# Optimization experiments

Hardware: AMD Instinct MI355X
Metric: run time of the kernel (lower is better)

The kernel has to match this reference:

```python
import jax, jax.numpy as jnp
import numpy as np

NUM_EXPERTS = 8
TOP_K = 2
N_EMBD = 1024
D_FFN = 2048  # 4*n_embd//top_k, already multiple of block_size=128


def setup_inputs() -> dict:
    key = jax.random.key(0)
    k1, k2, k3, k4 = jax.random.split(key, 4)
    x = jax.random.normal(k1, (4, 2048, N_EMBD), dtype=jnp.float32)
    router_w = jax.random.normal(k2, (NUM_EXPERTS, N_EMBD), dtype=jnp.float32) * 0.02
    w1 = jax.random.normal(k3, (N_EMBD, D_FFN * NUM_EXPERTS), dtype=jnp.float32) * 0.02
    w2 = jax.random.normal(k4, (D_FFN * NUM_EXPERTS, N_EMBD), dtype=jnp.float32) * 0.02
    return {"x": x, "router_w": router_w, "w1": w1, "w2": w2}


def reference(x, router_w, w1, w2):
    B, T, D = x.shape
    xf = x.reshape(B * T, D)                       # [N, d]
    N = B * T

    # Router: softmax over experts, then top-k selection and renormalization.
    logits = xf @ router_w.T                       # [N, E]
    probs = jax.nn.softmax(logits, axis=-1)
    top_v, top_i = jax.lax.top_k(probs, TOP_K)     # [N, k]
    top_v = top_v / jnp.sum(top_v, axis=-1, keepdims=True)  # norm_topk_prob=True

    # Dense [N, E] routing-weight matrix (zero for non-selected experts).
    gate = jnp.zeros((N, NUM_EXPERTS), dtype=x.dtype)
    gate = gate.at[jnp.arange(N)[:, None], top_i].set(top_v)

    w1r = w1.reshape(D, NUM_EXPERTS, D_FFN)        # expert-major column blocks
    w2r = w2.reshape(NUM_EXPERTS, D_FFN, D)

    out = jnp.zeros((N, D), dtype=x.dtype)
    for e in range(NUM_EXPERTS):
        h = jax.nn.gelu(xf @ w1r[:, e, :], approximate=False)  # [N, f]
        out = out + gate[:, e:e + 1] * (h @ w2r[e])
    return out.reshape(B, T, D)
```

## Files before the change

### kernel.cpp

```cpp
#include <hip/hip_runtime.h>
#include <hip/hip_bf16.h>
#include <cstdint>
#include <cstddef>

#define NE 8
#define N_TOK 8192
#define D_EMB 1024
#define D_FFN 2048

#define BM 128
#define BN 128
#define BK 32

typedef __attribute__((ext_vector_type(8))) short short8;
typedef __attribute__((ext_vector_type(4))) float f32x4;

__device__ __forceinline__ unsigned short f2bf(float f) {
  union { float f; unsigned int u; } c; c.f = f;
  unsigned int u = c.u;
  unsigned int r = u + 0x7FFFu + ((u >> 16) & 1u);
  return (unsigned short)(r >> 16);
}

__device__ __forceinline__ float bf2f(unsigned short u) {
  union { unsigned int u; float f; } c; c.u = ((unsigned int)u) << 16;
  return c.f;
}

__device__ __forceinline__ float gelu_f(float x) {
  float u = x * x * x * 0.044715f + x;
  float t = __expf(-1.5957691216057308f * u);
  return x * __builtin_amdgcn_rcpf(1.f + t);
}

__device__ __forceinline__ void gll16(const void* g, void* l) {
  __builtin_amdgcn_global_load_lds((const __attribute__((address_space(1))) void*)g,
                                   (__attribute__((address_space(3))) void*)l, 16, 0, 0);
}

#define SB() __builtin_amdgcn_sched_barrier(0)
#define VW(N) { asm volatile("s_waitcnt vmcnt(" #N ")" ::: "memory"); SB(); }
#define BAR() { SB(); __builtin_amdgcn_s_barrier(); SB(); }
#define LKW() { asm volatile("s_waitcnt lgkmcnt(0)" ::: "memory"); SB(); }

__global__ __launch_bounds__(256) void router_k(const float* __restrict__ x,
                                                const float* __restrict__ rw,
                                                int* __restrict__ ti,
                                                float* __restrict__ tg,
                                                ushort* __restrict__ xb) {
  int w = threadIdx.x >> 6, lane = threadIdx.x & 63;
  int n = blockIdx.x * 4 + w;
  const float4* x4 = (const float4*)(x + (size_t)n * D_EMB);
  ushort4* xb4 = (ushort4*)(xb + (size_t)n * D_EMB);
  const float4* r4 = (const float4*)rw;
  float acc[NE];
#pragma unroll
  for (int e = 0; e < NE; ++e) acc[e] = 0.f;
#pragma unroll
  for (int c = 0; c < 4; ++c) {
    float4 xv = x4[c * 64 + lane];
    ushort4 o;
    o.x = f2bf(xv.x); o.y = f2bf(xv.y); o.z = f2bf(xv.z); o.w = f2bf(xv.w);
    xb4[c * 64 + lane] = o;
#pragma unroll
    for (int e = 0; e < NE; ++e) {
      float4 wv = r4[e * 256 + c * 64 + lane];
      acc[e] += xv.x * wv.x + xv.y * wv.y + xv.z * wv.z + xv.w * wv.w;
    }
  }
#pragma unroll
  for (int e = 0; e < NE; ++e) {
    float v = acc[e];
#pragma unroll
    for (int off = 32; off >= 1; off >>= 1) v += __shfl_xor(v, off);
    acc[e] = v;
  }
  if (lane == 0) {
    int e0 = 0; float v0 = acc[0];
#pragma unroll
    for (int e = 1; e < NE; ++e) if (acc[e] > v0) { v0 = acc[e]; e0 = e; }
    int e1 = -1; float v1 = -1e30f;
#pragma unroll
    for (int e = 0; e < NE; ++e) if (e != e0 && acc[e] > v1) { v1 = acc[e]; e1 = e; }
    float p1 = expf(v1 - v0);
    float g0 = 1.f / (1.f + p1);
    float g1 = p1 * g0;
    ti[2 * n] = e0; ti[2 * n + 1] = e1;
    tg[2 * n] = g0; tg[2 * n + 1] = g1;
  }
}

__global__ __launch_bounds__(256) void prep_k(const float* __restrict__ w1,
                                              const float* __restrict__ w2,
                                              const int* __restrict__ ti,
                                              ushort* __restrict__ w1t,
                                              ushort* __restrict__ w2te,
                                              int* __restrict__ counts) {
  int b = blockIdx.x;
  if (b >= 32768) {
    __shared__ int lc[NE];
    if (threadIdx.x < NE) lc[threadIdx.x] = 0;
    __syncthreads();
    int s = (b - 32768) * 512 + threadIdx.x;
    atomicAdd(&lc[ti[s]], 1);
    atomicAdd(&lc[ti[s + 256]], 1);
    __syncthreads();
    if (threadIdx.x < NE) atomicAdd(&counts[threadIdx.x], lc[threadIdx.x]);
    return;
  }
  __shared__ ushort t[32][33];
  int rl = threadIdx.x >> 3, q = threadIdx.x & 7;
  if (b < 16384) {
    int bx = b & 511, by = b >> 9;
    const int C = NE * D_FFN;
    float4 v = *(const float4*)&w1[(size_t)(by * 32 + rl) * C + bx * 32 + q * 4];
    t[rl][q * 4 + 0] = f2bf(v.x);
    t[rl][q * 4 + 1] = f2bf(v.y);
    t[rl][q * 4 + 2] = f2bf(v.z);
    t[rl][q * 4 + 3] = f2bf(v.w);
    __syncthreads();
    ushort4 o;
    o.x = t[q * 4 + 0][rl];
    o.y = t[q * 4 + 1][rl];
    o.z = t[q * 4 + 2][rl];
    o.w = t[q * 4 + 3][rl];
    *(ushort4*)&w1t[(size_t)(bx * 32 + rl) * D_EMB + by * 32 + q * 4] = o;
  } else {
    int b2 = b - 16384;
    int bx = b2 & 31, by = b2 >> 5;
    float4 v = *(const float4*)&w2[(size_t)(by * 32 + rl) * D_EMB + bx * 32 + q * 4];
    t[rl][q * 4 + 0] = f2bf(v.x);
    t[rl][q * 4 + 1] = f2bf(v.y);
    t[rl][q * 4 + 2] = f2bf(v.z);
    t[rl][q * 4 + 3] = f2bf(v.w);
    __syncthreads();
    int e = by >> 6;
    int f0 = (by & 63) * 32;
    size_t eoff = (size_t)e * (D_EMB * D_FFN);
    ushort4 o;
    o.x = t[q * 4 + 0][rl];
    o.y = t[q * 4 + 1][rl];
    o.z = t[q * 4 + 2][rl];
    o.w = t[q * 4 + 3][rl];
    *(ushort4*)&w2te[eoff + (size_t)(bx * 32 + rl) * D_FFN + f0 + q * 4] = o;
  }
}

__global__ void prefix_k(const int* __restrict__ counts, int* __restrict__ bases,
                         int* __restrict__ cursor) {
  if (threadIdx.x == 0) {
    int s = 0;
    for (int e = 0; e < NE; ++e) { bases[e] = s; cursor[e] = s; s += counts[e]; }
  }
}

__global__ __launch_bounds__(256) void scatter_k(const int* __restrict__ ti,
                                                 const float* __restrict__ tg,
                                                 int* __restrict__ cursor,
                                                 int* __restrict__ tokS,
                                                 float* __restrict__ gate) {
  __shared__ int lc[NE], lb[NE];
  if (threadIdx.x < NE) lc[threadIdx.x] = 0;
  __syncthreads();
  int s = blockIdx.x * 256 + threadIdx.x;
  int e = ti[s];
  float g = tg[s];
  int loc = atomicAdd(&lc[e], 1);
  __syncthreads();
  if (threadIdx.x < NE) lb[threadIdx.x] = atomicAdd(&cursor[threadIdx.x], lc[threadIdx.x]);
  __syncthreads();
  int pos = lb[e] + loc;
  tokS[pos] = s;
  gate[pos] = g;
}


#define STG(BUF)                                                           \
  { _Pragma("unroll") for (int j_ = 0; j_ < 2; ++j_) {                     \
      gll16(aptr[j_], &Al[BUF][ldso[j_]]);                                 \
      gll16(bptr[j_], &Bl[BUF][ldso[j_]]);                                 \
      aptr[j_] += BK; bptr[j_] += BK;                                      \
    } }

#define CMP(BUF)                                                           \
  { short8 a[4], b[4];                                                     \
    _Pragma("unroll") for (int i_ = 0; i_ < 4; ++i_)                       \
      a[i_] = *(const short8*)&Al[BUF][arow + i_ * 16 * BK];               \
    _Pragma("unroll") for (int j_ = 0; j_ < 4; ++j_)                       \
      b[j_] = *(const short8*)&Bl[BUF][brow + j_ * 16 * BK];               \
    _Pragma("unroll") for (int i_ = 0; i_ < 4; ++i_)                       \
      _Pragma("unroll") for (int j_ = 0; j_ < 4; ++j_)                     \
        acc[i_][j_] = __builtin_amdgcn_mfma_f32_16x16x32_bf16(a[i_], b[j_], acc[i_][j_], 0, 0, 0); \
  }

#define KLOOP(NT)                                                          \
  STG(0);                                                                  \
  for (int ks = 0; ks < (NT) - 2; ks += 2) {                               \
    STG(1); VW(4); BAR(); CMP(0); BAR();                                   \
    STG(0); VW(4); BAR(); CMP(1); BAR();                                   \
  }                                                                        \
  STG(1); VW(4); BAR(); CMP(0); BAR();                                     \
  VW(0); BAR(); CMP(1);

__global__ __launch_bounds__(256) void gemm1_k(const ushort* __restrict__ xb,
                                               const ushort* __restrict__ w1t,
                                               const int* __restrict__ counts,
                                               const int* __restrict__ bases,
                                               const int* __restrict__ tokS,
                                               ushort* __restrict__ h) {
  int bid = (int)blockIdx.x;
  bid = (bid & 7) * 512 + (bid >> 3);
  int e = bid >> 9;
  int rem = bid & 511;
  int mt = rem >> 4, nt = rem & 15;
  int count = counts[e];
  if (mt * BM >= count) return;
  int base = bases[e];

  __shared__ ushort Al[2][BM * BK];
  __shared__ ushort Bl[2][BN * BK];

  int tid = threadIdx.x;
  int w = tid >> 6, lane = tid & 63;

  const int ssw = (((lane & 3) ^ ((lane >> 3) & 3))) * 8;

  const ushort* aptr[2]; const ushort* bptr[2];
  int ldso[2];
#pragma unroll
  for (int j = 0; j < 2; ++j) {
    int rl = w * 32 + j * 16 + (lane >> 2);
    int pr = min(base + mt * BM + rl, base + count - 1);
    int t = tokS[pr] >> 1;
    aptr[j] = xb + (size_t)t * D_EMB + ssw;
    int c = e * D_FFN + nt * BN + rl;
    bptr[j] = w1t + (size_t)c * D_EMB + ssw;
    ldso[j] = (w * 32 + j * 16) * BK;
  }

  f32x4 zero = {0.f, 0.f, 0.f, 0.f};
  f32x4 acc[4][4];
#pragma unroll
  for (int i = 0; i < 4; ++i)
#pragma unroll
    for (int j = 0; j < 4; ++j) acc[i][j] = zero;

  int wm = w >> 1, wn = w & 1;
  const int rsw = ((lane >> 4) ^ (((lane & 15) >> 1) & 3)) * 8;
  const int arow = (wm * 64 + (lane & 15)) * BK + rsw;
  const int brow = (wn * 64 + (lane & 15)) * BK + rsw;

  KLOOP(D_EMB / BK);

  __syncthreads();
  ushort* ep = &Bl[0][0] + w * (16 * 72);
  int r0 = mt * BM + wm * 64, c0 = nt * BN + wn * 64;
  const int l15 = lane & 15;
#pragma unroll
  for (int i = 0; i < 4; ++i) {
#pragma unroll
    for (int j = 0; j < 4; ++j)
#pragma unroll
      for (int q = 0; q < 4; ++q)
        ep[((lane >> 4) * 4 + q) * 72 + j * 16 + l15] = f2bf(gelu_f(acc[i][j][q]));
    LKW();
#pragma unroll
    for (int rd = 0; rd < 2; ++rd) {
      int sr = (lane >> 3) + rd * 8;
      int sc = (lane & 7) * 8;
      short8 v = *(const short8*)&ep[sr * 72 + sc];
      int row = r0 + i * 16 + sr;
      if (row < count)
        *(short8*)&h[(size_t)(base + row) * D_FFN + c0 + sc] = v;
    }
    LKW();
  }
}

__global__ __launch_bounds__(256) void gemm2_k(const ushort* __restrict__ h,
                                               const ushort* __restrict__ w2te,
                                               const int* __restrict__ counts,
                                               const int* __restrict__ bases,
                                               const int* __restrict__ tokS,
                                               const float* __restrict__ gate,
                                               ushort* __restrict__ y2) {
  int bid = (int)blockIdx.x;
  bid = (bid & 7) * 256 + (bid >> 3);
  int e = bid >> 8;
  int rem = bid & 255;
  int mt = rem >> 3, nt = rem & 7;
  int count = counts[e];
  if (mt * BM >= count) return;
  int base = bases[e];

  __shared__ ushort Al[2][BM * BK];
  __shared__ ushort Bl[2][BN * BK];

  int tid = threadIdx.x;
  int w = tid >> 6, lane = tid & 63;

  const int ssw = (((lane & 3) ^ ((lane >> 3) & 3))) * 8;

  const ushort* aptr[2]; const ushort* bptr[2];
  int ldso[2];
#pragma unroll
  for (int j = 0; j < 2; ++j) {
    int rl = w * 32 + j * 16 + (lane >> 2);
    int pr = min(base + mt * BM + rl, base + count - 1);
    aptr[j] = h + (size_t)pr * D_FFN + ssw;
    int d = nt * BN + rl;
    bptr[j] = w2te + (size_t)e * (D_EMB * D_FFN) + (size_t)d * D_FFN + ssw;
    ldso[j] = (w * 32 + j * 16) * BK;
  }

  f32x4 zero = {0.f, 0.f, 0.f, 0.f};
  f32x4 acc[4][4];
#pragma unroll
  for (int i = 0; i < 4; ++i)
#pragma unroll
    for (int j = 0; j < 4; ++j) acc[i][j] = zero;

  int wm = w >> 1, wn = w & 1;
  const int rsw = ((lane >> 4) ^ (((lane & 15) >> 1) & 3)) * 8;
  const int arow = (wm * 64 + (lane & 15)) * BK + rsw;
  const int brow = (wn * 64 + (lane & 15)) * BK + rsw;

  KLOOP(D_FFN / BK);

  __syncthreads();
  ushort* ep = &Bl[0][0] + w * (16 * 72);
  int r0 = mt * BM + wm * 64, c0 = nt * BN + wn * 64;
  const int l15 = lane & 15;
#pragma unroll
  for (int i = 0; i < 4; ++i) {
#pragma unroll
    for (int q = 0; q < 4; ++q) {
      int row = r0 + i * 16 + (lane >> 4) * 4 + q;
      int pr = min(base + row, base + count - 1);
      float g = gate[pr];
#pragma unroll
      for (int j = 0; j < 4; ++j)
        ep[((lane >> 4) * 4 + q) * 72 + j * 16 + l15] = f2bf(g * acc[i][j][q]);
    }
    LKW();
#pragma unroll
    for (int rd = 0; rd < 2; ++rd) {
      int sr = (lane >> 3) + rd * 8;
      int sc = (lane & 7) * 8;
      short8 v = *(const short8*)&ep[sr * 72 + sc];
      int row = r0 + i * 16 + sr;
      if (row < count) {
        int pr = base + row;
        *(short8*)&y2[(size_t)tokS[pr] * D_EMB + c0 + sc] = v;
      }
    }
    LKW();
  }
}

__global__ __launch_bounds__(256) void combine_k(const ushort* __restrict__ y2,
                                                 float* __restrict__ out) {
  int n = blockIdx.x;
  const ushort4* r0 = (const ushort4*)(y2 + (size_t)(2 * n) * D_EMB);
  const ushort4* r1 = (const ushort4*)(y2 + (size_t)(2 * n + 1) * D_EMB);
  float4* o = (float4*)(out + (size_t)n * D_EMB);
  int i = threadIdx.x;
  ushort4 a = r0[i], b = r1[i];
  float4 v;
  v.x = bf2f(a.x) + bf2f(b.x);
  v.y = bf2f(a.y) + bf2f(b.y);
  v.z = bf2f(a.z) + bf2f(b.z);
  v.w = bf2f(a.w) + bf2f(b.w);
  o[i] = v;
}

extern "C" void kernel_launch(void* const* d_in, const int* in_sizes, int n_in,
                              void* d_out, int out_size, void* d_ws, size_t ws_size,
                              hipStream_t stream) {
  const float* x  = (const float*)d_in[0];
  const float* rw = (const float*)d_in[1];
  const float* w1 = (const float*)d_in[2];
  const float* w2 = (const float*)d_in[3];
  float* out = (float*)d_out;

  char* ws = (char*)d_ws;
  size_t off = 0;
  auto alloc = [&](size_t bytes) {
    void* p = ws + off;
    off = (off + bytes + 255) & ~(size_t)255;
    return p;
  };
  int*    counts = (int*)alloc(32);
  int*    bases  = (int*)alloc(32);
  int*    cursor = (int*)alloc(32);
  int*    ti     = (int*)alloc((size_t)N_TOK * 2 * sizeof(int));
  float*  tg     = (float*)alloc((size_t)N_TOK * 2 * sizeof(float));
  int*    tokS   = (int*)alloc((size_t)N_TOK * 2 * sizeof(int));
  float*  gate   = (float*)alloc((size_t)N_TOK * 2 * sizeof(float));
  ushort* xb     = (ushort*)alloc((size_t)N_TOK * D_EMB * 2);
  ushort* w1t    = (ushort*)alloc((size_t)D_EMB * NE * D_FFN * 2);
  ushort* w2te   = (ushort*)alloc((size_t)D_EMB * NE * D_FFN * 2);
  ushort* hbuf   = (ushort*)alloc((size_t)N_TOK * 2 * D_FFN * 2);
  ushort* ybuf   = (ushort*)alloc((size_t)N_TOK * 2 * D_EMB * 2);
  (void)ws_size; (void)in_sizes; (void)n_in; (void)out_size;

  hipMemsetAsync(counts, 0, 32, stream);

  router_k<<<N_TOK / 4, 256, 0, stream>>>(x, rw, ti, tg, xb);
  prep_k<<<32800, 256, 0, stream>>>(w1, w2, ti, w1t, w2te, counts);
  prefix_k<<<1, 64, 0, stream>>>(counts, bases, cursor);
  scatter_k<<<N_TOK * 2 / 256, 256, 0, stream>>>(ti, tg, cursor, tokS, gate);
  gemm1_k<<<NE * 32 * 16, 256, 0, stream>>>(xb, w1t, counts, bases, tokS, hbuf);
  gemm2_k<<<NE * 32 * 8, 256, 0, stream>>>(hbuf, w2te, counts, bases, tokS, gate, ybuf);
  combine_k<<<N_TOK, 256, 0, stream>>>(ybuf, out);
}
```

Baseline: 274.5 us.

## Enlarge grouped GEMM tiles to 256x256 with 512-thread blocks

Both expert GEMMs move from 128x128 tiles with 4 waves to 256x256 tiles with 8 waves. Each wave now computes a 128x64 sub-tile with an 8x4 MFMA accumulator array. The LDS staging index math, swizzle and epilogue buffers are reworked to match, and the grid sizes shrink. The goal is more operand reuse per global load and less LDS traffic per FLOP. In exchange, register pressure rises, padding waste grows on ragged expert tails, and far fewer blocks are available to fill the CUs.

```diff
diff --git a/kernel.cpp b/kernel.cpp
--- a/kernel.cpp
+++ b/kernel.cpp
@@ -8,8 +8,8 @@
 #define D_EMB 1024
 #define D_FFN 2048
 
-#define BM 128
-#define BN 128
+#define BM 256
+#define BN 256
 #define BK 32
 
 typedef __attribute__((ext_vector_type(8))) short short8;
@@ -176,19 +176,19 @@
 
 
 #define STG(BUF)                                                           \
-  { _Pragma("unroll") for (int j_ = 0; j_ < 2; ++j_) {                     \
-      gll16(aptr[j_], &Al[BUF][ldso[j_]]);                                 \
-      gll16(bptr[j_], &Bl[BUF][ldso[j_]]);                                 \
-      aptr[j_] += BK; bptr[j_] += BK;                                      \
+  { _Pragma("unroll") for (int p_ = 0; p_ < 2; ++p_) {                     \
+      gll16(aptr[p_], &Al[BUF][p_ * 4096 + w * 512]);                      \
+      gll16(bptr[p_], &Bl[BUF][p_ * 4096 + w * 512]);                      \
+      aptr[p_] += BK; bptr[p_] += BK;                                      \
     } }
 
 #define CMP(BUF)                                                           \
-  { short8 a[4], b[4];                                                     \
-    _Pragma("unroll") for (int i_ = 0; i_ < 4; ++i_)                       \
+  { short8 a[8], b[4];                                                     \
+    _Pragma("unroll") for (int i_ = 0; i_ < 8; ++i_)                       \
       a[i_] = *(const short8*)&Al[BUF][arow + i_ * 16 * BK];               \
     _Pragma("unroll") for (int j_ = 0; j_ < 4; ++j_)                       \
       b[j_] = *(const short8*)&Bl[BUF][brow + j_ * 16 * BK];               \
-    _Pragma("unroll") for (int i_ = 0; i_ < 4; ++i_)                       \
+    _Pragma("unroll") for (int i_ = 0; i_ < 8; ++i_)                       \
       _Pragma("unroll") for (int j_ = 0; j_ < 4; ++j_)                     \
         acc[i_][j_] = __builtin_amdgcn_mfma_f32_16x16x32_bf16(a[i_], b[j_], acc[i_][j_], 0, 0, 0); \
   }
@@ -202,17 +202,17 @@
   STG(1); VW(4); BAR(); CMP(0); BAR();                                     \
   VW(0); BAR(); CMP(1);
 
-__global__ __launch_bounds__(256) void gemm1_k(const ushort* __restrict__ xb,
-                                               const ushort* __restrict__ w1t,
-                                               const int* __restrict__ counts,
-                                               const int* __restrict__ bases,
-                                               const int* __restrict__ tokS,
-                                               ushort* __restrict__ h) {
+__global__ __launch_bounds__(512, 2) void gemm1_k(const ushort* __restrict__ xb,
+                                                  const ushort* __restrict__ w1t,
+                                                  const int* __restrict__ counts,
+                                                  const int* __restrict__ bases,
+                                                  const int* __restrict__ tokS,
+                                                  ushort* __restrict__ h) {
   int bid = (int)blockIdx.x;
-  bid = (bid & 7) * 512 + (bid >> 3);
-  int e = bid >> 9;
-  int rem = bid & 511;
-  int mt = rem >> 4, nt = rem & 15;
+  bid = (bid & 7) * 128 + (bid >> 3);
+  int e = bid >> 7;
+  int rem = bid & 127;
+  int mt = rem >> 3, nt = rem & 7;
   int count = counts[e];
   if (mt * BM >= count) return;
   int base = bases[e];
@@ -222,42 +222,40 @@
 
   int tid = threadIdx.x;
   int w = tid >> 6, lane = tid & 63;
-
-  const int ssw = (((lane & 3) ^ ((lane >> 3) & 3))) * 8;
+  const int l15 = lane & 15;
+
+  const int ssw = (((tid & 3) ^ ((tid >> 3) & 3))) * 8;
 
   const ushort* aptr[2]; const ushort* bptr[2];
-  int ldso[2];
-#pragma unroll
-  for (int j = 0; j < 2; ++j) {
-    int rl = w * 32 + j * 16 + (lane >> 2);
-    int pr = min(base + mt * BM + rl, base + count - 1);
+#pragma unroll
+  for (int p = 0; p < 2; ++p) {
+    int R = p * 128 + (tid >> 2);
+    int pr = min(base + mt * BM + R, base + count - 1);
     int t = tokS[pr] >> 1;
-    aptr[j] = xb + (size_t)t * D_EMB + ssw;
-    int c = e * D_FFN + nt * BN + rl;
-    bptr[j] = w1t + (size_t)c * D_EMB + ssw;
-    ldso[j] = (w * 32 + j * 16) * BK;
+    aptr[p] = xb + (size_t)t * D_EMB + ssw;
+    int cB = e * D_FFN + nt * BN + R;
+    bptr[p] = w1t + (size_t)cB * D_EMB + ssw;
   }
 
   f32x4 zero = {0.f, 0.f, 0.f, 0.f};
-  f32x4 acc[4][4];
-#pragma unroll
-  for (int i = 0; i < 4; ++i)
+  f32x4 acc[8][4];
+#pragma unroll
+  for (int i = 0; i < 8; ++i)
 #pragma unroll
     for (int j = 0; j < 4; ++j) acc[i][j] = zero;
 
-  int wm = w >> 1, wn = w & 1;
-  const int rsw = ((lane >> 4) ^ (((lane & 15) >> 1) & 3)) * 8;
-  const int arow = (wm * 64 + (lane & 15)) * BK + rsw;
-  const int brow = (wn * 64 + (lane & 15)) * BK + rsw;
+  int wm = w >> 2, wn = w & 3;
+  const int rsw = ((lane >> 4) ^ ((l15 >> 1) & 3)) * 8;
+  const int arow = (wm * 128 + l15) * BK + rsw;
+  const int brow = (wn * 64 + l15) * BK + rsw;
 
   KLOOP(D_EMB / BK);
 
   __syncthreads();
-  ushort* ep = &Bl[0][0] + w * (16 * 72);
-  int r0 = mt * BM + wm * 64, c0 = nt * BN + wn * 64;
-  const int l15 = lane & 15;
-#pragma unroll
-  for (int i = 0; i < 4; ++i) {
+  ushort* ep = &Al[0][0] + w * 1152;
+  int r0 = mt * BM + wm * 128, c0 = nt * BN + wn * 64;
+#pragma unroll
+  for (int i = 0; i < 8; ++i) {
 #pragma unroll
     for (int j = 0; j < 4; ++j)
 #pragma unroll
@@ -277,18 +275,18 @@
   }
 }
 
-__global__ __launch_bounds__(256) void gemm2_k(const ushort* __restrict__ h,
-                                               const ushort* __restrict__ w2te,
-                                               const int* __restrict__ counts,
-                                               const int* __restrict__ bases,
-                                               const int* __restrict__ tokS,
-                                               const float* __restrict__ gate,
-                                               ushort* __restrict__ y2) {
+__global__ __launch_bounds__(512, 2) void gemm2_k(const ushort* __restrict__ h,
+                                                  const ushort* __restrict__ w2te,
+                                                  const int* __restrict__ counts,
+                                                  const int* __restrict__ bases,
+                                                  const int* __restrict__ tokS,
+                                                  const float* __restrict__ gate,
+                                                  ushort* __restrict__ y2) {
   int bid = (int)blockIdx.x;
-  bid = (bid & 7) * 256 + (bid >> 3);
-  int e = bid >> 8;
-  int rem = bid & 255;
-  int mt = rem >> 3, nt = rem & 7;
+  bid = (bid & 7) * 64 + (bid >> 3);
+  int e = bid >> 6;
+  int rem = bid & 63;
+  int mt = rem >> 2, nt = rem & 3;
   int count = counts[e];
   if (mt * BM >= count) return;
   int base = bases[e];
@@ -298,41 +296,39 @@
 
   int tid = threadIdx.x;
   int w = tid >> 6, lane = tid & 63;
-
-  const int ssw = (((lane & 3) ^ ((lane >> 3) & 3))) * 8;
+  const int l15 = lane & 15;
+
+  const int ssw = (((tid & 3) ^ ((tid >> 3) & 3))) * 8;
 
   const ushort* aptr[2]; const ushort* bptr[2];
-  int ldso[2];
-#pragma unroll
-  for (int j = 0; j < 2; ++j) {
-    int rl = w * 32 + j * 16 + (lane >> 2);
-    int pr = min(base + mt * BM + rl, base + count - 1);
-    aptr[j] = h + (size_t)pr * D_FFN + ssw;
-    int d = nt * BN + rl;
-    bptr[j] = w2te + (size_t)e * (D_EMB * D_FFN) + (size_t)d * D_FFN + ssw;
-    ldso[j] = (w * 32 + j * 16) * BK;
+#pragma unroll
+  for (int p = 0; p < 2; ++p) {
+    int R = p * 128 + (tid >> 2);
+    int pr = min(base + mt * BM + R, base + count - 1);
+    aptr[p] = h + (size_t)pr * D_FFN + ssw;
+    int d = nt * BN + R;
+    bptr[p] = w2te + (size_t)e * (D_EMB * D_FFN) + (size_t)d * D_FFN + ssw;
   }
 
   f32x4 zero = {0.f, 0.f, 0.f, 0.f};
-  f32x4 acc[4][4];
-#pragma unroll
-  for (int i = 0; i < 4; ++i)
+  f32x4 acc[8][4];
+#pragma unroll
+  for (int i = 0; i < 8; ++i)
 #pragma unroll
     for (int j = 0; j < 4; ++j) acc[i][j] = zero;
 
-  int wm = w >> 1, wn = w & 1;
-  const int rsw = ((lane >> 4) ^ (((lane & 15) >> 1) & 3)) * 8;
-  const int arow = (wm * 64 + (lane & 15)) * BK + rsw;
-  const int brow = (wn * 64 + (lane & 15)) * BK + rsw;
+  int wm = w >> 2, wn = w & 3;
+  const int rsw = ((lane >> 4) ^ ((l15 >> 1) & 3)) * 8;
+  const int arow = (wm * 128 + l15) * BK + rsw;
+  const int brow = (wn * 64 + l15) * BK + rsw;
 
   KLOOP(D_FFN / BK);
 
   __syncthreads();
-  ushort* ep = &Bl[0][0] + w * (16 * 72);
-  int r0 = mt * BM + wm * 64, c0 = nt * BN + wn * 64;
-  const int l15 = lane & 15;
-#pragma unroll
-  for (int i = 0; i < 4; ++i) {
+  ushort* ep = &Al[0][0] + w * 1152;
+  int r0 = mt * BM + wm * 128, c0 = nt * BN + wn * 64;
+#pragma unroll
+  for (int i = 0; i < 8; ++i) {
 #pragma unroll
     for (int q = 0; q < 4; ++q) {
       int row = r0 + i * 16 + (lane >> 4) * 4 + q;
@@ -410,7 +406,7 @@
   prep_k<<<32800, 256, 0, stream>>>(w1, w2, ti, w1t, w2te, counts);
   prefix_k<<<1, 64, 0, stream>>>(counts, bases, cursor);
   scatter_k<<<N_TOK * 2 / 256, 256, 0, stream>>>(ti, tg, cursor, tokS, gate);
-  gemm1_k<<<NE * 32 * 16, 256, 0, stream>>>(xb, w1t, counts, bases, tokS, hbuf);
-  gemm2_k<<<NE * 32 * 8, 256, 0, stream>>>(hbuf, w2te, counts, bases, tokS, gate, ybuf);
+  gemm1_k<<<NE * 16 * 8, 512, 0, stream>>>(xb, w1t, counts, bases, tokS, hbuf);
+  gemm2_k<<<NE * 16 * 4, 512, 0, stream>>>(hbuf, w2te, counts, bases, tokS, gate, ybuf);
   combine_k<<<N_TOK, 256, 0, stream>>>(ybuf, out);
 }
```

After: 301.2 us. +9.7%, slower.
